# Kernel tuning notes

Measured on AMD Instinct MI355X. Metric: run time of the kernel, lower is better.

Reference implementation:

```python
import jax, jax.numpy as jnp
import numpy as np

LEVELS = [(64, 64), (32, 32), (16, 16), (8, 8)]  # (H, W) per feature level
B, C, NH, NL, NP, NLAYERS, FFN = 8, 256, 8, 4, 4, 6, 1024
Q = sum(h * w for h, w in LEVELS)  # 5440
DH = C // NH


def setup_inputs() -> dict:
    key = jax.random.key(0)
    ks = iter(jax.random.split(key, 40))
    def rn(shape, s=0.02):
        return jax.random.normal(next(ks), shape, dtype=jnp.float32) * s
    return {
        'src_flat': jax.random.normal(next(ks), (B, Q, C), dtype=jnp.float32),
        'pos_flat': jax.random.normal(next(ks), (B, Q, C), dtype=jnp.float32) * 0.1,
        'level_embed': rn((NL, C), 0.1),
        'W_samp': rn((NLAYERS, C, NH * NL * NP * 2)),
        'b_samp': rn((NLAYERS, NH * NL * NP * 2), 0.1),
        'W_attn': rn((NLAYERS, C, NH * NL * NP)),
        'b_attn': rn((NLAYERS, NH * NL * NP), 0.1),
        'W_val': rn((NLAYERS, C, C)),
        'b_val': jnp.zeros((NLAYERS, C), jnp.float32),
        'W_out': rn((NLAYERS, C, C)),
        'b_out': jnp.zeros((NLAYERS, C), jnp.float32),
        'g1': jnp.ones((NLAYERS, C), jnp.float32),
        'b1': jnp.zeros((NLAYERS, C), jnp.float32),
        'W_fc1': rn((NLAYERS, C, FFN)),
        'b_fc1': jnp.zeros((NLAYERS, FFN), jnp.float32),
        'W_fc2': rn((NLAYERS, FFN, C)),
        'b_fc2': jnp.zeros((NLAYERS, C), jnp.float32),
        'g2': jnp.ones((NLAYERS, C), jnp.float32),
        'b2': jnp.zeros((NLAYERS, C), jnp.float32),
    }


def layer_norm(x, g, b):
    m = x.mean(-1, keepdims=True)
    v = ((x - m) ** 2).mean(-1, keepdims=True)
    return (x - m) * jax.lax.rsqrt(v + 1e-5) * g + b


def get_reference_points():
    # valid_ratios are all ones (masks are all-False), so ref pts are identical per level dim
    pts = []
    for (h, w) in LEVELS:
        ry = (jnp.arange(h, dtype=jnp.float32) + 0.5) / h
        rx = (jnp.arange(w, dtype=jnp.float32) + 0.5) / w
        yy, xx = jnp.meshgrid(ry, rx, indexing='ij')
        pts.append(jnp.stack([xx.ravel(), yy.ravel()], -1))
    return jnp.concatenate(pts, 0)  # [Q, 2] in (x, y)


def ms_deform_attn(query, src, ref_pts, Ws, bs, Wa, ba, Wv, bv, Wo, bo):
    value = (src @ Wv + bv).reshape(B, Q, NH, DH)
    off = (query @ Ws + bs).reshape(B, Q, NH, NL, NP, 2)
    aw = jax.nn.softmax((query @ Wa + ba).reshape(B, Q, NH, NL * NP), axis=-1)
    aw = aw.reshape(B, Q, NH, NL, NP).transpose(0, 2, 1, 3, 4)  # [B,NH,Q,NL,NP]
    normalizer = jnp.array([[w, h] for (h, w) in LEVELS], jnp.float32)  # (x, y) per level
    loc = ref_pts[None, :, None, None, None, :] + off / normalizer[None, None, None, :, None, :]
    out = jnp.zeros((B, NH, Q, DH), jnp.float32)
    start = 0
    for l, (h, w) in enumerate(LEVELS):
        v_l = value[:, start:start + h * w].transpose(0, 2, 1, 3)  # [B,NH,HW,DH]
        start += h * w
        loc_l = loc[:, :, :, l]  # [B,Q,NH,NP,2]
        x = loc_l[..., 0] * w - 0.5  # grid_sample align_corners=False pixel coords
        y = loc_l[..., 1] * h - 0.5
        x0 = jnp.floor(x)
        y0 = jnp.floor(y)
        fx = x - x0
        fy = y - y0
        sampled = jnp.zeros((B, NH, Q, NP, DH), jnp.float32)
        for dy, dx in ((0, 0), (0, 1), (1, 0), (1, 1)):
            cy = y0 + dy
            cx = x0 + dx
            wgt = (fy if dy else 1.0 - fy) * (fx if dx else 1.0 - fx)
            valid = (cy >= 0) & (cy < h) & (cx >= 0) & (cx < w)  # zero padding
            wgt = jnp.where(valid, wgt, 0.0)
            idx = (jnp.clip(cy, 0, h - 1) * w + jnp.clip(cx, 0, w - 1)).astype(jnp.int32)
            idx = idx.transpose(0, 2, 1, 3).reshape(B, NH, Q * NP)
            g = jnp.take_along_axis(v_l, idx[..., None], axis=2).reshape(B, NH, Q, NP, DH)
            sampled = sampled + g * wgt.transpose(0, 2, 1, 3)[..., None]
        out = out + (sampled * aw[:, :, :, l, :, None]).sum(3)
    out = out.transpose(0, 2, 1, 3).reshape(B, Q, C)
    return out @ Wo + bo


def reference(src_flat, pos_flat, level_embed, W_samp, b_samp, W_attn, b_attn, W_val, b_val, W_out, b_out, g1, b1, W_fc1, b_fc1, W_fc2, b_fc2, g2, b2):
    counts = np.array([h * w for h, w in LEVELS])
    lvl_emb = jnp.repeat(level_embed, counts, axis=0, total_repeat_length=Q)  # [Q,C]
    pos = pos_flat + lvl_emb[None]
    ref = get_reference_points()
    out = src_flat
    for i in range(NLAYERS):
        q = out + pos
        attn = ms_deform_attn(q, out, ref, W_samp[i], b_samp[i], W_attn[i], b_attn[i], W_val[i], b_val[i], W_out[i], b_out[i])
        out = layer_norm(out + attn, g1[i], b1[i])
        hid = jax.nn.relu(out @ W_fc1[i] + b_fc1[i]) @ W_fc2[i] + b_fc2[i]
        out = layer_norm(out + hid, g2[i], b2[i])
    return out
```

## Files before the change

### kernel.cpp

```cpp
#include <hip/hip_runtime.h>
#include <hip/hip_bf16.h>

#define NB 8
#define NC 256
#define NH_ 8
#define NLAYERS_ 6
#define FFN_ 1024
#define Q_ 5440
#define DH_ 32
#define M_ (NB*Q_)
#define MC2 (M_/2)

typedef __attribute__((ext_vector_type(8))) short bf16x8;
typedef __attribute__((ext_vector_type(4))) short bf16x4;
typedef __attribute__((ext_vector_type(4))) float f32x4;
typedef __attribute__((ext_vector_type(4))) int i32x4;
typedef __attribute__((ext_vector_type(4))) unsigned int u32x4;
typedef unsigned int u32;

__device__ __forceinline__ unsigned short f2bf(float f) {
  unsigned int u = __float_as_uint(f);
  u += 0x7fffu + ((u >> 16) & 1u);
  return (unsigned short)(u >> 16);
}
__device__ __forceinline__ float bf2f(unsigned short s) {
  return __uint_as_float(((unsigned int)s) << 16);
}
__device__ __forceinline__ void gl16(const unsigned short* g, unsigned short* l) {
  __builtin_amdgcn_global_load_lds((const __attribute__((address_space(1))) u32*)(g),
                                   (__attribute__((address_space(3))) u32*)(l), 16, 0, 0);
}
__device__ __forceinline__ void unp8(bf16x8 v, f32x4& lo, f32x4& hi) {
  u32x4 g = __builtin_bit_cast(u32x4, v);
  lo[0] = __uint_as_float(g[0] << 16); lo[1] = __uint_as_float(g[0] & 0xffff0000u);
  lo[2] = __uint_as_float(g[1] << 16); lo[3] = __uint_as_float(g[1] & 0xffff0000u);
  hi[0] = __uint_as_float(g[2] << 16); hi[1] = __uint_as_float(g[2] & 0xffff0000u);
  hi[2] = __uint_as_float(g[3] << 16); hi[3] = __uint_as_float(g[3] & 0xffff0000u);
}
__device__ __forceinline__ bf16x8 pck8(f32x4 lo, f32x4 hi) {
  bf16x8 o;
  o[0] = (short)f2bf(lo[0]); o[1] = (short)f2bf(lo[1]);
  o[2] = (short)f2bf(lo[2]); o[3] = (short)f2bf(lo[3]);
  o[4] = (short)f2bf(hi[0]); o[5] = (short)f2bf(hi[1]);
  o[6] = (short)f2bf(hi[2]); o[7] = (short)f2bf(hi[3]);
  return o;
}

__global__ void transpose_w2_k(const float* __restrict__ W, unsigned short* __restrict__ Wt,
                               int L, int Kd, int Nd, int NdTot, int nOff) {
  size_t total = (size_t)L * Nd * Kd;
  for (size_t i = (size_t)blockIdx.x * blockDim.x + threadIdx.x; i < total;
       i += (size_t)gridDim.x * blockDim.x) {
    int k = (int)(i % Kd);
    size_t r = i / Kd;
    int n = (int)(r % Nd);
    int l = (int)(r / Nd);
    Wt[((size_t)l * NdTot + nOff + n) * Kd + k] = f2bf(W[((size_t)l * Kd + k) * Nd + n]);
  }
}

__global__ void bias_cat_k(const float* __restrict__ bs, const float* __restrict__ ba,
                           float* __restrict__ bsa) {
  int i = blockIdx.x * blockDim.x + threadIdx.x;
  if (i >= NLAYERS_ * 384) return;
  int l = i / 384, n = i % 384;
  bsa[i] = (n < 256) ? bs[l * 256 + n] : ba[l * 128 + (n - 256)];
}

__global__ __launch_bounds__(256)
void pre_k(const float* __restrict__ src, const float* __restrict__ pf,
           const float* __restrict__ le, unsigned short* __restrict__ xb,
           unsigned short* __restrict__ pe, unsigned short* __restrict__ qb) {
  int row = blockIdx.x * 4 + (threadIdx.x >> 6);
  int lane = threadIdx.x & 63;
  size_t base = (size_t)row * NC + lane * 4;
  int q = row % Q_;
  int lvl = q < 4096 ? 0 : (q < 5120 ? 1 : (q < 5376 ? 2 : 3));
  f32x4 xv = *(const f32x4*)(src + base);
  f32x4 pv = *(const f32x4*)(pf + base) + *(const f32x4*)(le + lvl * NC + lane * 4);
  f32x4 qv = xv + pv;
  bf16x4 xo, po, qo;
#pragma unroll
  for (int j = 0; j < 4; ++j) {
    xo[j] = (short)f2bf(xv[j]); po[j] = (short)f2bf(pv[j]); qo[j] = (short)f2bf(qv[j]);
  }
  *(bf16x4*)(xb + base) = xo;
  *(bf16x4*)(pe + base) = po;
  *(bf16x4*)(qb + base) = qo;
}

__device__ __forceinline__ int swz(int r, int sl) { return sl ^ (r & 3) ^ ((r >> 2) & 3); }

#define ES 136
#define SHN 24576

__device__ __forceinline__ void gemm_body(const unsigned short* X, const unsigned short* Wt,
                                          const float* bias, unsigned short* Y,
                                          int Kdim, int Ndim, int n0, int m0,
                                          unsigned short* SH) {
  const int t = threadIdx.x;
  const int wave = t >> 6, lane = t & 63;
  const int wr = wave >> 1, wc = wave & 1;
  const int lr = lane & 15, lk = lane >> 4;
  const int r0 = t >> 2, sl0 = t & 3;
  const int r1 = (256 + t) >> 2;
  const int gs0 = swz(r0, sl0);
  const int gs1 = swz(r1, sl0);
  const unsigned short* xp0 = X + (size_t)(m0 + r0) * Kdim + gs0 * 8;
  const unsigned short* wp0 = Wt + (size_t)(n0 + r0) * Kdim + gs0 * 8;
  const unsigned short* xp1 = X + (size_t)(m0 + r1) * Kdim + gs1 * 8;
  const unsigned short* wp1 = Wt + (size_t)(n0 + r1) * Kdim + gs1 * 8;

  f32x4 acc[4][4];
#pragma unroll
  for (int i = 0; i < 4; ++i)
#pragma unroll
    for (int j = 0; j < 4; ++j)
#pragma unroll
      for (int e = 0; e < 4; ++e) acc[i][j][e] = 0.f;

  auto stage = [&](int buf, int kt) {
    unsigned short* base = SH + buf * 8192;
    gl16(xp0 + kt, base + t * 8);
    gl16(wp0 + kt, base + 4096 + t * 8);
    gl16(xp1 + kt, base + (256 + t) * 8);
    gl16(wp1 + kt, base + 4096 + (256 + t) * 8);
  };

  const int nt = Kdim >> 5;
  stage(0, 0);
  stage(1, 32);
  asm volatile("s_waitcnt vmcnt(4)" ::: "memory");
  __builtin_amdgcn_s_barrier();

  int buf = 0;
  for (int ti = 0; ti < nt; ++ti) {
    if (ti + 2 < nt) stage(buf == 0 ? 2 : buf - 1, (ti + 2) << 5);
    const unsigned short* Ab = SH + buf * 8192;
    const unsigned short* Bb = Ab + 4096;
    bf16x8 ar[4], br[4];
#pragma unroll
    for (int fi = 0; fi < 4; ++fi) {
      int r = wr * 64 + fi * 16 + lr;
      ar[fi] = *(const bf16x8*)&Ab[r * 32 + swz(r, lk) * 8];
    }
#pragma unroll
    for (int fj = 0; fj < 4; ++fj) {
      int r = wc * 64 + fj * 16 + lr;
      br[fj] = *(const bf16x8*)&Bb[r * 32 + swz(r, lk) * 8];
    }
#pragma unroll
    for (int fi = 0; fi < 4; ++fi)
#pragma unroll
      for (int fj = 0; fj < 4; ++fj)
        acc[fi][fj] = __builtin_amdgcn_mfma_f32_16x16x32_bf16(ar[fi], br[fj], acc[fi][fj], 0, 0, 0);
    if (ti + 2 < nt)
      asm volatile("s_waitcnt vmcnt(4)" ::: "memory");
    else
      asm volatile("s_waitcnt vmcnt(0)" ::: "memory");
    __builtin_amdgcn_s_barrier();
    buf = (buf == 2) ? 0 : buf + 1;
  }

#pragma unroll
  for (int fi = 0; fi < 4; ++fi)
#pragma unroll
    for (int fj = 0; fj < 4; ++fj) {
      int col = wc * 64 + fj * 16 + lr;
      float bv = bias[n0 + col];
#pragma unroll
      for (int rr = 0; rr < 4; ++rr) {
        int row = wr * 64 + fi * 16 + lk * 4 + rr;
        SH[row * ES + col] = f2bf(acc[fi][fj][rr] + bv);
      }
    }
  __syncthreads();
  {
    int row = t >> 1, hcol = (t & 1) * 64;
    const unsigned short* sp = SH + row * ES + hcol;
    unsigned short* dp = Y + (size_t)(m0 + row) * Ndim + n0 + hcol;
#pragma unroll
    for (int j = 0; j < 8; ++j)
      *(bf16x8*)(dp + j * 8) = *(const bf16x8*)(sp + j * 8);
  }
}

__global__ __launch_bounds__(256)
void gemm_vs_k(const unsigned short* __restrict__ X0, const unsigned short* __restrict__ W0,
               const float* __restrict__ b0, unsigned short* __restrict__ Y0,
               const unsigned short* __restrict__ X1, const unsigned short* __restrict__ W1,
               const float* __restrict__ b1, unsigned short* __restrict__ Y1) {
  __shared__ unsigned short SH[SHN];
  int bx = blockIdx.x, m0 = blockIdx.y * 128;
  if (bx < 2)
    gemm_body(X0, W0, b0, Y0, 256, 256, bx * 128, m0, SH);
  else
    gemm_body(X1, W1, b1, Y1, 256, 384, (bx - 2) * 128, m0, SH);
}

#define ESW 264
#define SH512 36864

template <int MODE>
__global__ __launch_bounds__(512, 4)
void gemm512_k(const unsigned short* __restrict__ X, const unsigned short* __restrict__ Wt,
               const float* __restrict__ bias, unsigned short* __restrict__ Y,
               const unsigned short* __restrict__ res, const float* __restrict__ g,
               const float* __restrict__ bta, const unsigned short* __restrict__ pe,
               unsigned short* __restrict__ out1, float* __restrict__ dout,
               int Kdim, int Ndim, int rowOff) {
  __shared__ unsigned short SH[SH512];
  const int t = threadIdx.x;
  int m0, n0, mOut;
  if constexpr (MODE == 0) {
    n0 = (blockIdx.x & 3) * 256;
    m0 = (blockIdx.x >> 2) * 128;
    mOut = m0;
  } else {
    n0 = 0;
    m0 = blockIdx.x * 128;
    mOut = rowOff + m0;
  }
  const int wave = t >> 6, lane = t & 63;
  const int wr = wave >> 2, wc = wave & 3;
  const int lr = lane & 15, lk = lane >> 4;
  const int rA = t >> 2, slA = t & 3;
  const int gsA = swz(rA, slA);
  const int rB1 = (512 + t) >> 2;
  const int gsB0 = gsA, gsB1 = swz(rB1, slA);
  const unsigned short* xp = X + (size_t)(m0 + rA) * Kdim + gsA * 8;
  const unsigned short* wp0 = Wt + (size_t)(n0 + rA) * Kdim + gsB0 * 8;
  const unsigned short* wp1 = Wt + (size_t)(n0 + rB1) * Kdim + gsB1 * 8;

  f32x4 acc[4][4];
#pragma unroll
  for (int i = 0; i < 4; ++i)
#pragma unroll
    for (int j = 0; j < 4; ++j)
#pragma unroll
      for (int e = 0; e < 4; ++e) acc[i][j][e] = 0.f;

  auto stage = [&](int buf, int kt) {
    unsigned short* base = SH + buf * 12288;
    gl16(xp + kt, base + t * 8);
    gl16(wp0 + kt, base + 4096 + t * 8);
    gl16(wp1 + kt, base + 4096 + (512 + t) * 8);
  };

  const int nt = Kdim >> 5;
  stage(0, 0);
  stage(1, 32);
  asm volatile("s_waitcnt vmcnt(3)" ::: "memory");
  __builtin_amdgcn_s_barrier();

  int buf = 0;
  for (int ti = 0; ti < nt; ++ti) {
    if (ti + 2 < nt) stage(buf == 0 ? 2 : buf - 1, (ti + 2) << 5);
    const unsigned short* Ab = SH + buf * 12288;
    const unsigned short* Bb = Ab + 4096;
    bf16x8 ar[4], br[4];
#pragma unroll
    for (int fi = 0; fi < 4; ++fi) {
      int r = wr * 64 + fi * 16 + lr;
      ar[fi] = *(const bf16x8*)&Ab[r * 32 + swz(r, lk) * 8];
    }
#pragma unroll
    for (int fj = 0; fj < 4; ++fj) {
      int r = wc * 64 + fj * 16 + lr;
      br[fj] = *(const bf16x8*)&Bb[r * 32 + swz(r, lk) * 8];
    }
#pragma unroll
    for (int fi = 0; fi < 4; ++fi)
#pragma unroll
      for (int fj = 0; fj < 4; ++fj)
        acc[fi][fj] = __builtin_amdgcn_mfma_f32_16x16x32_bf16(ar[fi], br[fj], acc[fi][fj], 0, 0, 0);
    if (ti + 2 < nt)
      asm volatile("s_waitcnt vmcnt(3)" ::: "memory");
    else
      asm volatile("s_waitcnt vmcnt(0)" ::: "memory");
    __builtin_amdgcn_s_barrier();
    buf = (buf == 2) ? 0 : buf + 1;
  }

#pragma unroll
  for (int fi = 0; fi < 4; ++fi)
#pragma unroll
    for (int fj = 0; fj < 4; ++fj) {
      int col = wc * 64 + fj * 16 + lr;
      float bv = bias[n0 + col];
#pragma unroll
      for (int rr = 0; rr < 4; ++rr) {
        int row = wr * 64 + fi * 16 + lk * 4 + rr;
        float v = acc[fi][fj][rr] + bv;
        if constexpr (MODE == 0) v = fmaxf(v, 0.f);
        SH[row * ESW + col] = f2bf(v);
      }
    }
  __syncthreads();

  const int row = t >> 2, seg = t & 3;
  const int c0 = seg * 64;
  const unsigned short* sp = SH + row * ESW + c0;

  if constexpr (MODE == 0) {
    unsigned short* dp = Y + (size_t)(mOut + row) * Ndim + n0 + c0;
#pragma unroll
    for (int j = 0; j < 8; ++j)
      *(bf16x8*)(dp + j * 8) = *(const bf16x8*)(sp + j * 8);
  } else {
    size_t rbase = (size_t)(mOut + row) * NC + c0;
    bf16x8 resv[8];
#pragma unroll
    for (int j = 0; j < 8; ++j) resv[j] = *(const bf16x8*)(res + rbase + j * 8);
    float sum = 0.f;
#pragma unroll
    for (int j = 0; j < 8; ++j) {
      f32x4 cl, ch, rl, rh;
      unp8(*(const bf16x8*)(sp + j * 8), cl, ch);
      unp8(resv[j], rl, rh);
      f32x4 a = cl + rl, b = ch + rh;
      sum += a[0] + a[1] + a[2] + a[3] + b[0] + b[1] + b[2] + b[3];
    }
    sum += __shfl_xor(sum, 1);
    sum += __shfl_xor(sum, 2);
    float mean = sum * (1.0f / NC);
    float s2 = 0.f;
#pragma unroll
    for (int j = 0; j < 8; ++j) {
      f32x4 cl, ch, rl, rh;
      unp8(*(const bf16x8*)(sp + j * 8), cl, ch);
      unp8(resv[j], rl, rh);
      f32x4 a = cl + rl - mean, b = ch + rh - mean;
      s2 += a[0]*a[0] + a[1]*a[1] + a[2]*a[2] + a[3]*a[3]
          + b[0]*b[0] + b[1]*b[1] + b[2]*b[2] + b[3]*b[3];
    }
    s2 += __shfl_xor(s2, 1);
    s2 += __shfl_xor(s2, 2);
    float rstd = rsqrtf(s2 * (1.0f / NC) + 1e-5f);
#pragma unroll
    for (int j = 0; j < 8; ++j) {
      int col = c0 + j * 8;
      f32x4 cl, ch, rl, rh;
      unp8(*(const bf16x8*)(sp + j * 8), cl, ch);
      unp8(resv[j], rl, rh);
      f32x4 gl = *(const f32x4*)(g + col), gh = *(const f32x4*)(g + col + 4);
      f32x4 bl = *(const f32x4*)(bta + col), bh = *(const f32x4*)(bta + col + 4);
      f32x4 ol = (cl + rl - mean) * rstd * gl + bl;
      f32x4 oh = (ch + rh - mean) * rstd * gh + bh;
      *(bf16x8*)(Y + rbase + j * 8) = pck8(ol, oh);
      if constexpr (MODE >= 2) {
        f32x4 pl, ph;
        unp8(*(const bf16x8*)(pe + rbase + j * 8), pl, ph);
        *(bf16x8*)(out1 + rbase + j * 8) = pck8(ol + pl, oh + ph);
      }
      if constexpr (MODE == 3) {
        *(f32x4*)(dout + rbase + j * 8) = ol;
        *(f32x4*)(dout + rbase + j * 8 + 4) = oh;
      }
    }
  }
}

__global__ __launch_bounds__(256)
void samp_k(const unsigned short* __restrict__ value, const unsigned short* __restrict__ sa,
            unsigned short* __restrict__ attn_feat) {
  __shared__ float lw[4][128][4];
  __shared__ int   la[4][128][4];
  const int wid = threadIdx.x >> 6, lane = threadIdx.x & 63;
  const int bq = blockIdx.x * 4 + wid;
  const int q = bq % Q_;
  const int b = bq / Q_;

  int lvl = q < 4096 ? 0 : (q < 5120 ? 1 : (q < 5376 ? 2 : 3));
  int qrem = q - (lvl == 0 ? 0 : lvl == 1 ? 4096 : lvl == 2 ? 5120 : 5376);
  int wlog = 6 - lvl;
  float inv = __uint_as_float((unsigned)(127 - wlog) << 23);
  float refx = ((qrem & ((1 << wlog) - 1)) + 0.5f) * inv;
  float refy = ((qrem >> wlog) + 0.5f) * inv;
  const unsigned short* sa_bq = sa + (size_t)bq * 384;

  const int h_s = lane >> 3;
  const int s0 = (lane & 7) * 2;
  unsigned lg01 = *(const unsigned*)&sa_bq[256 + h_s * 16 + s0];
  float lg0 = bf2f((unsigned short)(lg01 & 0xffff));
  float lg1 = bf2f((unsigned short)(lg01 >> 16));
  float mx = fmaxf(lg0, lg1);
  mx = fmaxf(mx, __shfl_xor(mx, 1));
  mx = fmaxf(mx, __shfl_xor(mx, 2));
  mx = fmaxf(mx, __shfl_xor(mx, 4));
  float e0 = __expf(lg0 - mx), e1 = __expf(lg1 - mx);
  float sm = e0 + e1;
  sm += __shfl_xor(sm, 1);
  sm += __shfl_xor(sm, 2);
  sm += __shfl_xor(sm, 4);
  float rs = 1.0f / sm;

#pragma unroll
  for (int j = 0; j < 2; ++j) {
    int s = s0 + j;
    float aw = (j ? e1 : e0) * rs;
    unsigned oxy = *(const unsigned*)&sa_bq[h_s * 32 + s * 2];
    float ox = bf2f((unsigned short)(oxy & 0xffff));
    float oy = bf2f((unsigned short)(oxy >> 16));
    int sl = s >> 2;
    int swl = 6 - sl;
    int sw = 1 << swl;
    int sstart = (sl == 0) ? 0 : (sl == 1) ? 4096 : (sl == 2) ? 5120 : 5376;
    float x = fmaf(refx, (float)sw, ox) - 0.5f;
    float y = fmaf(refy, (float)sw, oy) - 0.5f;
    float x0f = floorf(x), y0f = floorf(y);
    float fx = x - x0f, fy = y - y0f;
    int x0 = (int)x0f, y0 = (int)y0f;
    int rowbase = b * Q_ + sstart;
    f32x4 wv; i32x4 av;
#pragma unroll
    for (int c = 0; c < 4; ++c) {
      int dy = c >> 1, dx = c & 1;
      int cy = y0 + dy, cx = x0 + dx;
      float wgt = (dy ? fy : 1.f - fy) * (dx ? fx : 1.f - fx);
      bool valid = (cy >= 0) & (cy < sw) & (cx >= 0) & (cx < sw);
      wgt = valid ? wgt : 0.f;
      int ccy = min(max(cy, 0), sw - 1);
      int ccx = min(max(cx, 0), sw - 1);
      wv[c] = wgt * aw;
      av[c] = ((rowbase + (ccy << swl) + ccx) * NH_ + h_s) * DH_;
    }
    int idx = s * 8 + (h_s ^ (s & 7));
    *(f32x4*)&lw[wid][idx][0] = wv;
    *(i32x4*)&la[wid][idx][0] = av;
  }
  __syncthreads();

  const int h = lane >> 3;
  const int half = (lane >> 2) & 1;
  const int quad = lane & 3;
  const unsigned short* vq = value + quad * 8;
  f32x4 accA = {0.f, 0.f, 0.f, 0.f}, accB = {0.f, 0.f, 0.f, 0.f};
#pragma unroll
  for (int i = 0; i < 8; ++i) {
    int s = half * 8 + i;
    int idx = s * 8 + (h ^ (s & 7));
    f32x4 wv = *(const f32x4*)&lw[wid][idx][0];
    i32x4 av = *(const i32x4*)&la[wid][idx][0];
#pragma unroll
    for (int c = 0; c < 4; ++c) {
      u32x4 gg = *(const u32x4*)(vq + av[c]);
      f32x4 v0, v1;
      v0[0] = __uint_as_float(gg[0] << 16); v0[1] = __uint_as_float(gg[0] & 0xffff0000u);
      v0[2] = __uint_as_float(gg[1] << 16); v0[3] = __uint_as_float(gg[1] & 0xffff0000u);
      v1[0] = __uint_as_float(gg[2] << 16); v1[1] = __uint_as_float(gg[2] & 0xffff0000u);
      v1[2] = __uint_as_float(gg[3] << 16); v1[3] = __uint_as_float(gg[3] & 0xffff0000u);
      float wcc = wv[c];
      accA += v0 * wcc;
      accB += v1 * wcc;
    }
  }
#pragma unroll
  for (int j = 0; j < 4; ++j) {
    accA[j] += __shfl_xor(accA[j], 4);
    accB[j] += __shfl_xor(accB[j], 4);
  }
  if (half == 0) {
    *(bf16x8*)(attn_feat + (size_t)bq * NC + h * DH_ + quad * 8) = pck8(accA, accB);
  }
}

extern "C" void kernel_launch(void* const* d_in, const int* in_sizes, int n_in,
                              void* d_out, int out_size, void* d_ws, size_t ws_size,
                              hipStream_t stream) {
  const float* src      = (const float*)d_in[0];
  const float* pos_flat = (const float*)d_in[1];
  const float* lvl_emb  = (const float*)d_in[2];
  const float* W_samp   = (const float*)d_in[3];
  const float* b_samp   = (const float*)d_in[4];
  const float* W_attn   = (const float*)d_in[5];
  const float* b_attn   = (const float*)d_in[6];
  const float* W_val    = (const float*)d_in[7];
  const float* b_val    = (const float*)d_in[8];
  const float* W_out    = (const float*)d_in[9];
  const float* b_out    = (const float*)d_in[10];
  const float* g1       = (const float*)d_in[11];
  const float* b1       = (const float*)d_in[12];
  const float* W_fc1    = (const float*)d_in[13];
  const float* b_fc1    = (const float*)d_in[14];
  const float* W_fc2    = (const float*)d_in[15];
  const float* b_fc2    = (const float*)d_in[16];
  const float* g2       = (const float*)d_in[17];
  const float* b2       = (const float*)d_in[18];

  char* ws = (char*)d_ws;
  size_t o = 0;
  auto alloc = [&](size_t bytes) {
    void* p = ws + o;
    o += (bytes + 255) & ~(size_t)255;
    return p;
  };
  unsigned short* bb    = (unsigned short*)alloc((size_t)MC2 * FFN_ * 2);
  unsigned short* sa    = (unsigned short*)alloc((size_t)M_ * 384 * 2);
  unsigned short* af    = (unsigned short*)alloc((size_t)M_ * NC * 2);
  unsigned short* xb    = (unsigned short*)alloc((size_t)M_ * NC * 2);
  unsigned short* xm    = (unsigned short*)alloc((size_t)M_ * NC * 2);
  unsigned short* qb    = (unsigned short*)alloc((size_t)M_ * NC * 2);
  unsigned short* pe    = (unsigned short*)alloc((size_t)M_ * NC * 2);
  unsigned short* Wv_t  = (unsigned short*)alloc((size_t)6 * 256 * 256 * 2);
  unsigned short* Wsa_t = (unsigned short*)alloc((size_t)6 * 384 * 256 * 2);
  unsigned short* Wo_t  = (unsigned short*)alloc((size_t)6 * 256 * 256 * 2);
  unsigned short* Wf1_t = (unsigned short*)alloc((size_t)6 * 1024 * 256 * 2);
  unsigned short* Wf2_t = (unsigned short*)alloc((size_t)6 * 256 * 1024 * 2);
  float* bsa            = (float*)alloc((size_t)6 * 384 * 4);

  transpose_w2_k<<<1536, 256, 0, stream>>>(W_val, Wv_t, 6, 256, 256, 256, 0);
  transpose_w2_k<<<1536, 256, 0, stream>>>(W_samp, Wsa_t, 6, 256, 256, 384, 0);
  transpose_w2_k<<<768, 256, 0, stream>>>(W_attn, Wsa_t, 6, 256, 128, 384, 256);
  transpose_w2_k<<<1536, 256, 0, stream>>>(W_out, Wo_t, 6, 256, 256, 256, 0);
  transpose_w2_k<<<3072, 256, 0, stream>>>(W_fc1, Wf1_t, 6, 256, 1024, 1024, 0);
  transpose_w2_k<<<3072, 256, 0, stream>>>(W_fc2, Wf2_t, 6, 1024, 256, 256, 0);
  bias_cat_k<<<9, 256, 0, stream>>>(b_samp, b_attn, bsa);
  pre_k<<<M_ / 4, 256, 0, stream>>>(src, pos_flat, lvl_emb, xb, pe, qb);

  for (int i = 0; i < NLAYERS_; ++i) {
    gemm_vs_k<<<dim3(5, M_ / 128), 256, 0, stream>>>(
        xb, Wv_t + (size_t)i * 65536, b_val + i * 256, bb,
        qb, Wsa_t + (size_t)i * 98304, bsa + i * 384, sa);
    samp_k<<<M_ / 4, 256, 0, stream>>>(bb, sa, af);
    gemm512_k<1><<<M_ / 128, 512, 0, stream>>>(
        af, Wo_t + (size_t)i * 65536, b_out + i * 256, xm,
        xb, g1 + i * 256, b1 + i * 256, nullptr, nullptr, nullptr, 256, 256, 0);
    for (int c = 0; c < 2; ++c) {
      int rowOff = c * MC2;
      gemm512_k<0><<<(MC2 / 128) * 4, 512, 0, stream>>>(
          xm + (size_t)rowOff * NC, Wf1_t + (size_t)i * 262144, b_fc1 + i * 1024, bb,
          nullptr, nullptr, nullptr, nullptr, nullptr, nullptr, 256, 1024, 0);
      if (i == NLAYERS_ - 1)
        gemm512_k<3><<<MC2 / 128, 512, 0, stream>>>(
            bb, Wf2_t + (size_t)i * 262144, b_fc2 + i * 256, xb,
            xm, g2 + i * 256, b2 + i * 256, pe, qb, (float*)d_out, 1024, 256, rowOff);
      else
        gemm512_k<2><<<MC2 / 128, 512, 0, stream>>>(
            bb, Wf2_t + (size_t)i * 262144, b_fc2 + i * 256, xb,
            xm, g2 + i * 256, b2 + i * 256, pe, qb, nullptr, 1024, 256, rowOff);
    }
  }
}
```

Baseline: 1.778 ms.

## Use 4-wave blocks with 64x128 warp tiles in the 128x256 GEMMs

Result: no change. 1.772 ms (-0.3%).

```diff
diff --git a/kernel.cpp b/kernel.cpp
--- a/kernel.cpp
+++ b/kernel.cpp
@@ -199,58 +199,54 @@
 }
 
 #define ESW 264
-#define SH512 36864
+#define SHW 36864
 
 template <int MODE>
-__global__ __launch_bounds__(512, 4)
-void gemm512_k(const unsigned short* __restrict__ X, const unsigned short* __restrict__ Wt,
-               const float* __restrict__ bias, unsigned short* __restrict__ Y,
-               const unsigned short* __restrict__ res, const float* __restrict__ g,
-               const float* __restrict__ bta, const unsigned short* __restrict__ pe,
-               unsigned short* __restrict__ out1, float* __restrict__ dout,
-               int Kdim, int Ndim, int rowOff) {
-  __shared__ unsigned short SH[SH512];
+__global__ __launch_bounds__(256, 2)
+void gemmW_k(const unsigned short* __restrict__ X, const unsigned short* __restrict__ Wt,
+             const float* __restrict__ bias, unsigned short* __restrict__ Y,
+             const unsigned short* __restrict__ res, const float* __restrict__ g,
+             const float* __restrict__ bta, const unsigned short* __restrict__ pe,
+             unsigned short* __restrict__ out1, float* __restrict__ dout,
+             int Kdim, int Ndim, int rowOff) {
+  __shared__ unsigned short SH[SHW];
   const int t = threadIdx.x;
-  int m0, n0, mOut;
-  if constexpr (MODE == 0) {
-    n0 = (blockIdx.x & 3) * 256;
-    m0 = (blockIdx.x >> 2) * 128;
-    mOut = m0;
-  } else {
-    n0 = 0;
-    m0 = blockIdx.x * 128;
-    mOut = rowOff + m0;
-  }
+  const int n0 = blockIdx.x * 256;
+  const int m0 = blockIdx.y * 128;
+  const int mOut = rowOff + m0;
   const int wave = t >> 6, lane = t & 63;
-  const int wr = wave >> 2, wc = wave & 3;
+  const int wr = wave >> 1, wc = wave & 1;
   const int lr = lane & 15, lk = lane >> 4;
-  const int rA = t >> 2, slA = t & 3;
-  const int gsA = swz(rA, slA);
-  const int rB1 = (512 + t) >> 2;
-  const int gsB0 = gsA, gsB1 = swz(rB1, slA);
-  const unsigned short* xp = X + (size_t)(m0 + rA) * Kdim + gsA * 8;
-  const unsigned short* wp0 = Wt + (size_t)(n0 + rA) * Kdim + gsB0 * 8;
-  const unsigned short* wp1 = Wt + (size_t)(n0 + rB1) * Kdim + gsB1 * 8;
-
-  f32x4 acc[4][4];
+  const int rs = t >> 2, sl0 = t & 3;
+  const unsigned short* xpA0 = X + (size_t)(m0 + rs) * Kdim + swz(rs, sl0) * 8;
+  const unsigned short* xpA1 = X + (size_t)(m0 + 64 + rs) * Kdim + swz(64 + rs, sl0) * 8;
+  const unsigned short* wpB0 = Wt + (size_t)(n0 + rs) * Kdim + swz(rs, sl0) * 8;
+  const unsigned short* wpB1 = Wt + (size_t)(n0 + 64 + rs) * Kdim + swz(64 + rs, sl0) * 8;
+  const unsigned short* wpB2 = Wt + (size_t)(n0 + 128 + rs) * Kdim + swz(128 + rs, sl0) * 8;
+  const unsigned short* wpB3 = Wt + (size_t)(n0 + 192 + rs) * Kdim + swz(192 + rs, sl0) * 8;
+
+  f32x4 acc[4][8];
 #pragma unroll
   for (int i = 0; i < 4; ++i)
 #pragma unroll
-    for (int j = 0; j < 4; ++j)
+    for (int j = 0; j < 8; ++j)
 #pragma unroll
       for (int e = 0; e < 4; ++e) acc[i][j][e] = 0.f;
 
   auto stage = [&](int buf, int kt) {
     unsigned short* base = SH + buf * 12288;
-    gl16(xp + kt, base + t * 8);
-    gl16(wp0 + kt, base + 4096 + t * 8);
-    gl16(wp1 + kt, base + 4096 + (512 + t) * 8);
+    gl16(xpA0 + kt, base + t * 8);
+    gl16(xpA1 + kt, base + (256 + t) * 8);
+    gl16(wpB0 + kt, base + 4096 + t * 8);
+    gl16(wpB1 + kt, base + 4096 + (256 + t) * 8);
+    gl16(wpB2 + kt, base + 4096 + (512 + t) * 8);
+    gl16(wpB3 + kt, base + 4096 + (768 + t) * 8);
   };
 
   const int nt = Kdim >> 5;
   stage(0, 0);
   stage(1, 32);
-  asm volatile("s_waitcnt vmcnt(3)" ::: "memory");
+  asm volatile("s_waitcnt vmcnt(6)" ::: "memory");
   __builtin_amdgcn_s_barrier();
 
   int buf = 0;
@@ -258,24 +254,24 @@
     if (ti + 2 < nt) stage(buf == 0 ? 2 : buf - 1, (ti + 2) << 5);
     const unsigned short* Ab = SH + buf * 12288;
     const unsigned short* Bb = Ab + 4096;
-    bf16x8 ar[4], br[4];
+    bf16x8 ar[4], br[8];
 #pragma unroll
     for (int fi = 0; fi < 4; ++fi) {
       int r = wr * 64 + fi * 16 + lr;
       ar[fi] = *(const bf16x8*)&Ab[r * 32 + swz(r, lk) * 8];
     }
 #pragma unroll
-    for (int fj = 0; fj < 4; ++fj) {
-      int r = wc * 64 + fj * 16 + lr;
+    for (int fj = 0; fj < 8; ++fj) {
+      int r = wc * 128 + fj * 16 + lr;
       br[fj] = *(const bf16x8*)&Bb[r * 32 + swz(r, lk) * 8];
     }
 #pragma unroll
     for (int fi = 0; fi < 4; ++fi)
 #pragma unroll
-      for (int fj = 0; fj < 4; ++fj)
+      for (int fj = 0; fj < 8; ++fj)
         acc[fi][fj] = __builtin_amdgcn_mfma_f32_16x16x32_bf16(ar[fi], br[fj], acc[fi][fj], 0, 0, 0);
     if (ti + 2 < nt)
-      asm volatile("s_waitcnt vmcnt(3)" ::: "memory");
+      asm volatile("s_waitcnt vmcnt(6)" ::: "memory");
     else
       asm volatile("s_waitcnt vmcnt(0)" ::: "memory");
     __builtin_amdgcn_s_barrier();
@@ -285,8 +281,8 @@
 #pragma unroll
   for (int fi = 0; fi < 4; ++fi)
 #pragma unroll
-    for (int fj = 0; fj < 4; ++fj) {
-      int col = wc * 64 + fj * 16 + lr;
+    for (int fj = 0; fj < 8; ++fj) {
+      int col = wc * 128 + fj * 16 + lr;
       float bv = bias[n0 + col];
 #pragma unroll
       for (int rr = 0; rr < 4; ++rr) {
@@ -298,23 +294,23 @@
     }
   __syncthreads();
 
-  const int row = t >> 2, seg = t & 3;
-  const int c0 = seg * 64;
+  const int row = t >> 1;
+  const int c0 = (t & 1) * 128;
   const unsigned short* sp = SH + row * ESW + c0;
 
   if constexpr (MODE == 0) {
-    unsigned short* dp = Y + (size_t)(mOut + row) * Ndim + n0 + c0;
-#pragma unroll
-    for (int j = 0; j < 8; ++j)
+    unsigned short* dp = Y + (size_t)(m0 + row) * Ndim + n0 + c0;
+#pragma unroll
+    for (int j = 0; j < 16; ++j)
       *(bf16x8*)(dp + j * 8) = *(const bf16x8*)(sp + j * 8);
   } else {
     size_t rbase = (size_t)(mOut + row) * NC + c0;
-    bf16x8 resv[8];
-#pragma unroll
-    for (int j = 0; j < 8; ++j) resv[j] = *(const bf16x8*)(res + rbase + j * 8);
+    bf16x8 resv[16];
+#pragma unroll
+    for (int j = 0; j < 16; ++j) resv[j] = *(const bf16x8*)(res + rbase + j * 8);
     float sum = 0.f;
 #pragma unroll
-    for (int j = 0; j < 8; ++j) {
+    for (int j = 0; j < 16; ++j) {
       f32x4 cl, ch, rl, rh;
       unp8(*(const bf16x8*)(sp + j * 8), cl, ch);
       unp8(resv[j], rl, rh);
@@ -322,11 +318,10 @@
       sum += a[0] + a[1] + a[2] + a[3] + b[0] + b[1] + b[2] + b[3];
     }
     sum += __shfl_xor(sum, 1);
-    sum += __shfl_xor(sum, 2);
     float mean = sum * (1.0f / NC);
     float s2 = 0.f;
 #pragma unroll
-    for (int j = 0; j < 8; ++j) {
+    for (int j = 0; j < 16; ++j) {
       f32x4 cl, ch, rl, rh;
       unp8(*(const bf16x8*)(sp + j * 8), cl, ch);
       unp8(resv[j], rl, rh);
@@ -335,10 +330,9 @@
           + b[0]*b[0] + b[1]*b[1] + b[2]*b[2] + b[3]*b[3];
     }
     s2 += __shfl_xor(s2, 1);
-    s2 += __shfl_xor(s2, 2);
     float rstd = rsqrtf(s2 * (1.0f / NC) + 1e-5f);
 #pragma unroll
-    for (int j = 0; j < 8; ++j) {
+    for (int j = 0; j < 16; ++j) {
       int col = c0 + j * 8;
       f32x4 cl, ch, rl, rh;
       unp8(*(const bf16x8*)(sp + j * 8), cl, ch);
@@ -523,20 +517,20 @@
         xb, Wv_t + (size_t)i * 65536, b_val + i * 256, bb,
         qb, Wsa_t + (size_t)i * 98304, bsa + i * 384, sa);
     samp_k<<<M_ / 4, 256, 0, stream>>>(bb, sa, af);
-    gemm512_k<1><<<M_ / 128, 512, 0, stream>>>(
+    gemmW_k<1><<<dim3(1, M_ / 128), 256, 0, stream>>>(
         af, Wo_t + (size_t)i * 65536, b_out + i * 256, xm,
         xb, g1 + i * 256, b1 + i * 256, nullptr, nullptr, nullptr, 256, 256, 0);
     for (int c = 0; c < 2; ++c) {
       int rowOff = c * MC2;
-      gemm512_k<0><<<(MC2 / 128) * 4, 512, 0, stream>>>(
+      gemmW_k<0><<<dim3(4, MC2 / 128), 256, 0, stream>>>(
           xm + (size_t)rowOff * NC, Wf1_t + (size_t)i * 262144, b_fc1 + i * 1024, bb,
           nullptr, nullptr, nullptr, nullptr, nullptr, nullptr, 256, 1024, 0);
       if (i == NLAYERS_ - 1)
-        gemm512_k<3><<<MC2 / 128, 512, 0, stream>>>(
+        gemmW_k<3><<<dim3(1, MC2 / 128), 256, 0, stream>>>(
             bb, Wf2_t + (size_t)i * 262144, b_fc2 + i * 256, xb,
             xm, g2 + i * 256, b2 + i * 256, pe, qb, (float*)d_out, 1024, 256, rowOff);
       else
-        gemm512_k<2><<<MC2 / 128, 512, 0, stream>>>(
+        gemmW_k<2><<<dim3(1, MC2 / 128), 256, 0, stream>>>(
             bb, Wf2_t + (size_t)i * 262144, b_fc2 + i * 256, xb,
             xm, g2 + i * 256, b2 + i * 256, pe, qb, nullptr, 1024, 256, rowOff);
     }
```

## Shrink GEMM tiles to 64x256 with 256 threads and remap sampling blocks

Applied to the files above, without the earlier changes.

Result: no change. 1.785 ms (+0.4%).

```diff
diff --git a/kernel.cpp b/kernel.cpp
--- a/kernel.cpp
+++ b/kernel.cpp
@@ -199,38 +199,30 @@
 }
 
 #define ESW 264
-#define SH512 36864
+#define SHW 30720
 
 template <int MODE>
-__global__ __launch_bounds__(512, 4)
-void gemm512_k(const unsigned short* __restrict__ X, const unsigned short* __restrict__ Wt,
-               const float* __restrict__ bias, unsigned short* __restrict__ Y,
-               const unsigned short* __restrict__ res, const float* __restrict__ g,
-               const float* __restrict__ bta, const unsigned short* __restrict__ pe,
-               unsigned short* __restrict__ out1, float* __restrict__ dout,
-               int Kdim, int Ndim, int rowOff) {
-  __shared__ unsigned short SH[SH512];
+__global__ __launch_bounds__(256)
+void gemmW_k(const unsigned short* __restrict__ X, const unsigned short* __restrict__ Wt,
+             const float* __restrict__ bias, unsigned short* __restrict__ Y,
+             const unsigned short* __restrict__ res, const float* __restrict__ g,
+             const float* __restrict__ bta, const unsigned short* __restrict__ pe,
+             unsigned short* __restrict__ out1, float* __restrict__ dout,
+             int Kdim, int Ndim, int rowOff) {
+  __shared__ unsigned short SH[SHW];
   const int t = threadIdx.x;
-  int m0, n0, mOut;
-  if constexpr (MODE == 0) {
-    n0 = (blockIdx.x & 3) * 256;
-    m0 = (blockIdx.x >> 2) * 128;
-    mOut = m0;
-  } else {
-    n0 = 0;
-    m0 = blockIdx.x * 128;
-    mOut = rowOff + m0;
-  }
-  const int wave = t >> 6, lane = t & 63;
-  const int wr = wave >> 2, wc = wave & 3;
+  const int n0 = (MODE == 0) ? blockIdx.x * 256 : 0;
+  const int m0 = blockIdx.y * 64;
+  const int mOut = rowOff + m0;
+  const int wc = t >> 6;
+  const int lane = t & 63;
   const int lr = lane & 15, lk = lane >> 4;
-  const int rA = t >> 2, slA = t & 3;
-  const int gsA = swz(rA, slA);
-  const int rB1 = (512 + t) >> 2;
-  const int gsB0 = gsA, gsB1 = swz(rB1, slA);
-  const unsigned short* xp = X + (size_t)(m0 + rA) * Kdim + gsA * 8;
-  const unsigned short* wp0 = Wt + (size_t)(n0 + rA) * Kdim + gsB0 * 8;
-  const unsigned short* wp1 = Wt + (size_t)(n0 + rB1) * Kdim + gsB1 * 8;
+  const int rs = t >> 2, sl0 = t & 3;
+  const unsigned short* xpA  = X + (size_t)(m0 + rs) * Kdim + swz(rs, sl0) * 8;
+  const unsigned short* wpB0 = Wt + (size_t)(n0 + rs) * Kdim + swz(rs, sl0) * 8;
+  const unsigned short* wpB1 = Wt + (size_t)(n0 + 64 + rs) * Kdim + swz(64 + rs, sl0) * 8;
+  const unsigned short* wpB2 = Wt + (size_t)(n0 + 128 + rs) * Kdim + swz(128 + rs, sl0) * 8;
+  const unsigned short* wpB3 = Wt + (size_t)(n0 + 192 + rs) * Kdim + swz(192 + rs, sl0) * 8;
 
   f32x4 acc[4][4];
 #pragma unroll
@@ -241,27 +233,29 @@
       for (int e = 0; e < 4; ++e) acc[i][j][e] = 0.f;
 
   auto stage = [&](int buf, int kt) {
-    unsigned short* base = SH + buf * 12288;
-    gl16(xp + kt, base + t * 8);
-    gl16(wp0 + kt, base + 4096 + t * 8);
-    gl16(wp1 + kt, base + 4096 + (512 + t) * 8);
+    unsigned short* base = SH + buf * 10240;
+    gl16(xpA + kt, base + t * 8);
+    gl16(wpB0 + kt, base + 2048 + t * 8);
+    gl16(wpB1 + kt, base + 2048 + (256 + t) * 8);
+    gl16(wpB2 + kt, base + 2048 + (512 + t) * 8);
+    gl16(wpB3 + kt, base + 2048 + (768 + t) * 8);
   };
 
   const int nt = Kdim >> 5;
   stage(0, 0);
   stage(1, 32);
-  asm volatile("s_waitcnt vmcnt(3)" ::: "memory");
+  asm volatile("s_waitcnt vmcnt(5)" ::: "memory");
   __builtin_amdgcn_s_barrier();
 
   int buf = 0;
   for (int ti = 0; ti < nt; ++ti) {
     if (ti + 2 < nt) stage(buf == 0 ? 2 : buf - 1, (ti + 2) << 5);
-    const unsigned short* Ab = SH + buf * 12288;
-    const unsigned short* Bb = Ab + 4096;
+    const unsigned short* Ab = SH + buf * 10240;
+    const unsigned short* Bb = Ab + 2048;
     bf16x8 ar[4], br[4];
 #pragma unroll
     for (int fi = 0; fi < 4; ++fi) {
-      int r = wr * 64 + fi * 16 + lr;
+      int r = fi * 16 + lr;
       ar[fi] = *(const bf16x8*)&Ab[r * 32 + swz(r, lk) * 8];
     }
 #pragma unroll
@@ -275,7 +269,7 @@
       for (int fj = 0; fj < 4; ++fj)
         acc[fi][fj] = __builtin_amdgcn_mfma_f32_16x16x32_bf16(ar[fi], br[fj], acc[fi][fj], 0, 0, 0);
     if (ti + 2 < nt)
-      asm volatile("s_waitcnt vmcnt(3)" ::: "memory");
+      asm volatile("s_waitcnt vmcnt(5)" ::: "memory");
     else
       asm volatile("s_waitcnt vmcnt(0)" ::: "memory");
     __builtin_amdgcn_s_barrier();
@@ -290,7 +284,7 @@
       float bv = bias[n0 + col];
 #pragma unroll
       for (int rr = 0; rr < 4; ++rr) {
-        int row = wr * 64 + fi * 16 + lk * 4 + rr;
+        int row = fi * 16 + lk * 4 + rr;
         float v = acc[fi][fj][rr] + bv;
         if constexpr (MODE == 0) v = fmaxf(v, 0.f);
         SH[row * ESW + col] = f2bf(v);
@@ -298,12 +292,12 @@
     }
   __syncthreads();
 
-  const int row = t >> 2, seg = t & 3;
-  const int c0 = seg * 64;
+  const int row = t >> 2;
+  const int c0 = (t & 3) * 64;
   const unsigned short* sp = SH + row * ESW + c0;
 
   if constexpr (MODE == 0) {
-    unsigned short* dp = Y + (size_t)(mOut + row) * Ndim + n0 + c0;
+    unsigned short* dp = Y + (size_t)(m0 + row) * Ndim + n0 + c0;
 #pragma unroll
     for (int j = 0; j < 8; ++j)
       *(bf16x8*)(dp + j * 8) = *(const bf16x8*)(sp + j * 8);
@@ -366,8 +360,10 @@
             unsigned short* __restrict__ attn_feat) {
   __shared__ float lw[4][128][4];
   __shared__ int   la[4][128][4];
+  const int bid = blockIdx.x;
+  const int sbid = (bid & 7) * 1360 + (bid >> 3);
   const int wid = threadIdx.x >> 6, lane = threadIdx.x & 63;
-  const int bq = blockIdx.x * 4 + wid;
+  const int bq = sbid * 4 + wid;
   const int q = bq % Q_;
   const int b = bq / Q_;
 
@@ -523,20 +519,20 @@
         xb, Wv_t + (size_t)i * 65536, b_val + i * 256, bb,
         qb, Wsa_t + (size_t)i * 98304, bsa + i * 384, sa);
     samp_k<<<M_ / 4, 256, 0, stream>>>(bb, sa, af);
-    gemm512_k<1><<<M_ / 128, 512, 0, stream>>>(
+    gemmW_k<1><<<dim3(1, M_ / 64), 256, 0, stream>>>(
         af, Wo_t + (size_t)i * 65536, b_out + i * 256, xm,
         xb, g1 + i * 256, b1 + i * 256, nullptr, nullptr, nullptr, 256, 256, 0);
     for (int c = 0; c < 2; ++c) {
       int rowOff = c * MC2;
-      gemm512_k<0><<<(MC2 / 128) * 4, 512, 0, stream>>>(
+      gemmW_k<0><<<dim3(4, MC2 / 64), 256, 0, stream>>>(
           xm + (size_t)rowOff * NC, Wf1_t + (size_t)i * 262144, b_fc1 + i * 1024, bb,
           nullptr, nullptr, nullptr, nullptr, nullptr, nullptr, 256, 1024, 0);
       if (i == NLAYERS_ - 1)
-        gemm512_k<3><<<MC2 / 128, 512, 0, stream>>>(
+        gemmW_k<3><<<dim3(1, MC2 / 64), 256, 0, stream>>>(
             bb, Wf2_t + (size_t)i * 262144, b_fc2 + i * 256, xb,
             xm, g2 + i * 256, b2 + i * 256, pe, qb, (float*)d_out, 1024, 256, rowOff);
       else
-        gemm512_k<2><<<MC2 / 128, 512, 0, stream>>>(
+        gemmW_k<2><<<dim3(1, MC2 / 64), 256, 0, stream>>>(
             bb, Wf2_t + (size_t)i * 262144, b_fc2 + i * 256, xb,
             xm, g2 + i * 256, b2 + i * 256, pe, qb, nullptr, 1024, 256, rowOff);
     }
```
